# Kernel tuning notes

Measured on AMD Instinct MI355X. Metric: run time of the kernel, lower is better.

Reference implementation:

```python
import jax, jax.numpy as jnp
import numpy as np

T, H, F, E, K = 1024, 1024, 2048, 8, 2  # tokens, hidden, ffn_inter, experts, top_k


def setup_inputs() -> dict:
    key = jax.random.key(0)
    ks = jax.random.split(key, 7)
    return {
        "hidden_states": jax.random.normal(ks[0], (T, H), dtype=jnp.float32),
        "token_selected_experts": jax.random.randint(ks[1], (T, K), 0, E, dtype=jnp.int32),
        "token_final_scales": jax.random.uniform(ks[2], (T, K), dtype=jnp.float32),
        "w1": jax.random.normal(ks[3], (E, 2 * F, H), dtype=jnp.float32) * 0.02,  # gated fc1: [gate; linear]
        "b1": jax.random.normal(ks[4], (E, 2 * F), dtype=jnp.float32) * 0.02,
        "w2": jax.random.normal(ks[5], (E, H, F), dtype=jnp.float32) * 0.02,
        "b2": jax.random.normal(ks[6], (E, H), dtype=jnp.float32) * 0.02,
    }


def reference(hidden_states, token_selected_experts, token_final_scales, w1, b1, w2, b2):
    # Grouped GEMM fc1 over all experts: [T, E, 2F]
    h1 = jnp.einsum('th,efh->tef', hidden_states, w1) + b1[None]
    ffn = w2.shape[2]
    gate, lin = h1[..., :ffn], h1[..., ffn:]
    act = jax.nn.silu(gate) * lin                      # swiglu gated activation, [T, E, F]
    y_all = jnp.einsum('tef,ehf->teh', act, w2) + b2[None]  # fc2, [T, E, H]
    # Gather the top-k selected experts per token and combine with final scales
    sel = token_selected_experts.astype(jnp.int32)     # [T, K]
    y_sel = jnp.take_along_axis(y_all, sel[:, :, None], axis=1)  # [T, K, H]
    out = jnp.sum(y_sel * token_final_scales[:, :, None], axis=1)  # [T, H]
    return out
```

## Files before the change

### kernel.cpp

```cpp
#include <hip/hip_runtime.h>
#include <hip/hip_bf16.h>
#include <cstdint>
#include <cstddef>

#define TDIM 1024
#define HDIM 1024
#define FDIM 2048
#define NEXP 8
#define NENT 2048

typedef __bf16 bf16_t;
typedef __bf16 bf16x4 __attribute__((ext_vector_type(4)));
typedef __bf16 bf16x8 __attribute__((ext_vector_type(8)));
typedef float  f32x4  __attribute__((ext_vector_type(4)));

#define H_ELEMS ((size_t)TDIM*HDIM)

#define WB_OFFSETS 0
#define WB_ETOK    64
#define WB_ESCALE  (WB_ETOK + NENT*4)
#define WB_ACT     16512
#define WB_H       (WB_ACT + (size_t)NENT*FDIM*2)

__device__ __forceinline__ void gload16(const void* g, void* l) {
  __builtin_amdgcn_global_load_lds((const __attribute__((address_space(1))) void*)g,
                                   (__attribute__((address_space(3))) void*)l, 16, 0, 0);
}

__device__ __forceinline__ bf16x8 cvt8(const float4 a, const float4 b) {
  bf16x8 o;
  o[0]=(bf16_t)a.x; o[1]=(bf16_t)a.y; o[2]=(bf16_t)a.z; o[3]=(bf16_t)a.w;
  o[4]=(bf16_t)b.x; o[5]=(bf16_t)b.y; o[6]=(bf16_t)b.z; o[7]=(bf16_t)b.w;
  return o;
}

__global__ void route_all(const int* __restrict__ sel, const float* __restrict__ scal,
                          int* __restrict__ offsets, int* __restrict__ etok,
                          float* __restrict__ escale) {
  __shared__ int cnt[NEXP], cnt2[NEXP], offs[NEXP+1];
  const int t = threadIdx.x;
  if (t < NEXP) { cnt[t] = 0; cnt2[t] = 0; }
  __syncthreads();
  int e8[8];
  #pragma unroll
  for (int q = 0; q < 8; q++) {
    int i = t*8 + q;
    e8[q] = sel[i];
    atomicAdd(&cnt[e8[q]], 1);
  }
  __syncthreads();
  if (t == 0) {
    int s = 0;
    for (int e = 0; e < NEXP; e++) { offs[e] = s; offsets[e] = s; s += cnt[e]; }
    offs[NEXP] = s; offsets[NEXP] = s;
  }
  __syncthreads();
  #pragma unroll
  for (int q = 0; q < 8; q++) {
    int i = t*8 + q;
    int e = e8[q];
    int pos = offs[e] + atomicAdd(&cnt2[e], 1);
    etok[pos]   = i >> 1;
    escale[pos] = scal[i];
  }
}

__global__ void convert_h(const float* __restrict__ h, bf16_t* __restrict__ hbf) {
  size_t idx = ((size_t)blockIdx.x*256 + threadIdx.x) * 8;
  float4 v0 = ((const float4*)(h + idx))[0];
  float4 v1 = ((const float4*)(h + idx))[1];
  *(bf16x8*)(hbf + idx) = cvt8(v0, v1);
}


__global__ __launch_bounds__(256, 3) void gemm1_v5(
    const bf16_t* __restrict__ hbf, const float* __restrict__ w1,
    const float* __restrict__ b1, const int* __restrict__ offsets,
    const int* __restrict__ etok, bf16_t* __restrict__ act)
{
  const int e   = blockIdx.z;
  const int off = offsets[e];
  const int nt  = offsets[e+1] - off;
  const int m0  = blockIdx.y * 128;
  if (m0 >= nt) return;
  const int n0  = blockIdx.x * 64;

  __shared__ __align__(16) bf16_t As[128*32];
  __shared__ __align__(16) bf16_t Bg[64*32];
  __shared__ __align__(16) bf16_t Bl[64*32];

  const int tid  = threadIdx.x;
  const int w    = tid >> 6, lane = tid & 63;
  const int quad = lane >> 4, lr = lane & 15;
  const int wm   = w >> 1,  wn = w & 1;

  const bf16_t* asrc[2];
  bf16_t* adst[2];
  #pragma unroll
  for (int i = 0; i < 2; i++) {
    const int row = i*64 + w*16 + (lane >> 2);
    const int seg = (lane & 3) ^ (row & 3);
    int ent = m0 + row; if (ent > nt-1) ent = nt-1;
    const int tok = etok[off + ent];
    asrc[i] = hbf + (size_t)tok*HDIM + seg*8;
    adst[i] = &As[(i*64 + w*16)*32];
  }

  const int br = tid >> 2, bs = tid & 3;
  const float* gsrc = w1 + ((size_t)e*2*FDIM + (size_t)(n0 + br))*HDIM + bs*8;
  const float* lsrc = gsrc + (size_t)FDIM*HDIM;
  const int bofs = br*32 + ((bs ^ (br & 3)) << 3);

  const int aswz = (quad ^ (lr & 3)) << 3;
  int aoff[4], boff[2];
  #pragma unroll
  for (int i = 0; i < 4; i++) aoff[i] = (wm*64 + i*16 + lr)*32 + aswz;
  #pragma unroll
  for (int j = 0; j < 2; j++) boff[j] = (wn*32 + j*16 + lr)*32 + aswz;

  f32x4 accg[4][2] = {}, accl[4][2] = {};

  float4 g4[2], l4[2];
  { const float4* p = (const float4*)gsrc; g4[0]=p[0]; g4[1]=p[1];
    const float4* q = (const float4*)lsrc; l4[0]=q[0]; l4[1]=q[1]; }

  for (int k0 = 0; k0 < HDIM; k0 += 32) {
    __syncthreads();
    gload16(asrc[0] + k0, adst[0]);
    gload16(asrc[1] + k0, adst[1]);
    *(bf16x8*)&Bg[bofs] = cvt8(g4[0], g4[1]);
    *(bf16x8*)&Bl[bofs] = cvt8(l4[0], l4[1]);
    __syncthreads();

    if (k0 + 32 < HDIM) {
      const float4* p = (const float4*)(gsrc + k0 + 32); g4[0]=p[0]; g4[1]=p[1];
      const float4* q = (const float4*)(lsrc + k0 + 32); l4[0]=q[0]; l4[1]=q[1];
    }

    bf16x8 af[4], gf[2], lf[2];
    #pragma unroll
    for (int i = 0; i < 4; i++) af[i] = *(const bf16x8*)&As[aoff[i]];
    #pragma unroll
    for (int j = 0; j < 2; j++) {
      gf[j] = *(const bf16x8*)&Bg[boff[j]];
      lf[j] = *(const bf16x8*)&Bl[boff[j]];
    }
    #pragma unroll
    for (int i = 0; i < 4; i++)
      #pragma unroll
      for (int j = 0; j < 2; j++) {
        accg[i][j] = __builtin_amdgcn_mfma_f32_16x16x32_bf16(af[i], gf[j], accg[i][j], 0, 0, 0);
        accl[i][j] = __builtin_amdgcn_mfma_f32_16x16x32_bf16(af[i], lf[j], accl[i][j], 0, 0, 0);
      }
  }

  #pragma unroll
  for (int j = 0; j < 2; j++) {
    const int f = n0 + wn*32 + j*16 + lr;
    const float bg_ = b1[e*2*FDIM + f];
    const float bl_ = b1[e*2*FDIM + FDIM + f];
    #pragma unroll
    for (int i = 0; i < 4; i++) {
      #pragma unroll
      for (int r = 0; r < 4; r++) {
        const int m = wm*64 + i*16 + quad*4 + r;
        if (m0 + m < nt) {
          const float g = accg[i][j][r] + bg_;
          const float l = accl[i][j][r] + bl_;
          const float s = g / (1.f + __expf(-g)) * l;
          act[(size_t)(off + m0 + m)*FDIM + f] = (bf16_t)s;
        }
      }
    }
  }
}

__global__ __launch_bounds__(256, 3) void gemm2_v5(
    const bf16_t* __restrict__ act, const float* __restrict__ w2,
    const float* __restrict__ b2, const int* __restrict__ offsets,
    const int* __restrict__ etok, const float* __restrict__ escale,
    float* __restrict__ out)
{
  const int e   = blockIdx.z;
  const int off = offsets[e];
  const int nt  = offsets[e+1] - off;
  const int m0  = blockIdx.y * 128;
  if (m0 >= nt) return;
  const int n0  = (blockIdx.x >> 2) * 128;
  const int kc  = blockIdx.x & 3;
  const int kbeg = kc * (FDIM/4);

  __shared__ __align__(16) bf16_t As[128*32];
  __shared__ __align__(16) bf16_t Bs[128*32];

  const int tid  = threadIdx.x;
  const int w    = tid >> 6, lane = tid & 63;
  const int quad = lane >> 4, lr = lane & 15;
  const int wm   = w >> 1,  wn = w & 1;

  const bf16_t* asrc[2];
  bf16_t* adst[2];
  #pragma unroll
  for (int i = 0; i < 2; i++) {
    const int row = i*64 + w*16 + (lane >> 2);
    const int seg = (lane & 3) ^ (row & 3);
    int ent = m0 + row; if (ent > nt-1) ent = nt-1;
    asrc[i] = act + (size_t)(off + ent)*FDIM + kbeg + seg*8;
    adst[i] = &As[(i*64 + w*16)*32];
  }

  const int br = tid >> 1, bc = tid & 1;
  const float* bsrc = w2 + ((size_t)e*HDIM + (size_t)(n0 + br))*FDIM + kbeg + bc*16;
  const int bofs0 = br*32 + (((2*bc)   ^ (br & 3)) << 3);
  const int bofs1 = br*32 + (((2*bc+1) ^ (br & 3)) << 3);

  const int aswz = (quad ^ (lr & 3)) << 3;
  int aoff[4], boff[4];
  #pragma unroll
  for (int i = 0; i < 4; i++) aoff[i] = (wm*64 + i*16 + lr)*32 + aswz;
  #pragma unroll
  for (int j = 0; j < 4; j++) boff[j] = (wn*64 + j*16 + lr)*32 + aswz;

  f32x4 acc[4][4] = {};

  float4 b4[4];
  { const float4* p = (const float4*)bsrc;
    b4[0]=p[0]; b4[1]=p[1]; b4[2]=p[2]; b4[3]=p[3]; }

  for (int k0 = 0; k0 < FDIM/4; k0 += 32) {
    __syncthreads();
    gload16(asrc[0] + k0, adst[0]);
    gload16(asrc[1] + k0, adst[1]);
    *(bf16x8*)&Bs[bofs0] = cvt8(b4[0], b4[1]);
    *(bf16x8*)&Bs[bofs1] = cvt8(b4[2], b4[3]);
    __syncthreads();

    if (k0 + 32 < FDIM/4) {
      const float4* p = (const float4*)(bsrc + k0 + 32);
      b4[0]=p[0]; b4[1]=p[1]; b4[2]=p[2]; b4[3]=p[3];
    }

    bf16x8 af[4], bfr[4];
    #pragma unroll
    for (int i = 0; i < 4; i++) af[i] = *(const bf16x8*)&As[aoff[i]];
    #pragma unroll
    for (int j = 0; j < 4; j++) bfr[j] = *(const bf16x8*)&Bs[boff[j]];
    #pragma unroll
    for (int i = 0; i < 4; i++)
      #pragma unroll
      for (int j = 0; j < 4; j++)
        acc[i][j] = __builtin_amdgcn_mfma_f32_16x16x32_bf16(af[i], bfr[j], acc[i][j], 0, 0, 0);
  }

  #pragma unroll
  for (int i = 0; i < 4; i++) {
    #pragma unroll
    for (int r = 0; r < 4; r++) {
      const int m = wm*64 + i*16 + quad*4 + r;
      if (m0 + m < nt) {
        const int slot = off + m0 + m;
        const int t    = etok[slot];
        const float s  = escale[slot];
        #pragma unroll
        for (int j = 0; j < 4; j++) {
          const int n = n0 + wn*64 + j*16 + lr;
          float v = acc[i][j][r];
          if (kc == 0) v += b2[e*HDIM + n];
          atomicAdd(&out[(size_t)t*HDIM + n], s * v);
        }
      }
    }
  }
}

extern "C" void kernel_launch(void* const* d_in, const int* in_sizes, int n_in,
                              void* d_out, int out_size, void* d_ws, size_t ws_size,
                              hipStream_t stream) {
  const float* hidden = (const float*)d_in[0];
  const int*   sel    = (const int*)d_in[1];
  const float* scal   = (const float*)d_in[2];
  const float* w1     = (const float*)d_in[3];
  const float* b1     = (const float*)d_in[4];
  const float* w2     = (const float*)d_in[5];
  const float* b2     = (const float*)d_in[6];
  float* out = (float*)d_out;

  char* ws = (char*)d_ws;
  int*    offsets = (int*)(ws + WB_OFFSETS);
  int*    etok    = (int*)(ws + WB_ETOK);
  float*  escale  = (float*)(ws + WB_ESCALE);
  bf16_t* act     = (bf16_t*)(ws + WB_ACT);
  bf16_t* hbf     = (bf16_t*)(ws + WB_H);

  hipMemsetAsync(d_out, 0, (size_t)out_size * sizeof(float), stream);

  route_all<<<1, 256, 0, stream>>>(sel, scal, offsets, etok, escale);
  convert_h<<<(int)(H_ELEMS/8/256), 256, 0, stream>>>(hidden, hbf);

  gemm1_v5<<<dim3(FDIM/64, NENT/128, NEXP), 256, 0, stream>>>(hbf, w1, b1, offsets, etok, act);
  gemm2_v5<<<dim3((HDIM/128)*4, NENT/128, NEXP), 256, 0, stream>>>(act, w2, b2, offsets, etok, escale, out);
}
```

Baseline: 334.6 us.

## Double-buffer LDS tiles in both expert GEMMs with one barrier per step

Both grouped GEMM kernels now keep two LDS buffers for the A and B tiles. The next tile is staged (async global-to-LDS for activations, converted fp32 weights for B) while MFMAs run on the current one, and the two __syncthreads per k-step become a single s_barrier with explicit waitcnt and sched_barrier fences. The LDS swizzle also gains an extra XOR term on (row>>2)&3 to reduce bank conflicts. LDS use doubles, which may limit residency at 3 blocks per CU, and the hand-written vmcnt counts must match the issued loads exactly.

Measured after the change: 341.9 us. +2.2%, slower.

```diff
diff --git a/kernel.cpp b/kernel.cpp
--- a/kernel.cpp
+++ b/kernel.cpp
@@ -32,6 +32,10 @@
   o[0]=(bf16_t)a.x; o[1]=(bf16_t)a.y; o[2]=(bf16_t)a.z; o[3]=(bf16_t)a.w;
   o[4]=(bf16_t)b.x; o[5]=(bf16_t)b.y; o[6]=(bf16_t)b.z; o[7]=(bf16_t)b.w;
   return o;
+}
+
+__device__ __forceinline__ int segswz(int seg, int row) {
+  return seg ^ (row & 3) ^ ((row >> 2) & 3);
 }
 
 __global__ void route_all(const int* __restrict__ sel, const float* __restrict__ scal,
@@ -73,7 +77,7 @@
 }
 
 
-__global__ __launch_bounds__(256, 3) void gemm1_v5(
+__global__ __launch_bounds__(256, 3) void gemm1_v6(
     const bf16_t* __restrict__ hbf, const float* __restrict__ w1,
     const float* __restrict__ b1, const int* __restrict__ offsets,
     const int* __restrict__ etok, bf16_t* __restrict__ act)
@@ -85,74 +89,121 @@
   if (m0 >= nt) return;
   const int n0  = blockIdx.x * 64;
 
-  __shared__ __align__(16) bf16_t As[128*32];
-  __shared__ __align__(16) bf16_t Bg[64*32];
-  __shared__ __align__(16) bf16_t Bl[64*32];
+  __shared__ __align__(16) bf16_t As[2][128*32];
+  __shared__ __align__(16) bf16_t Bg[2][64*32];
+  __shared__ __align__(16) bf16_t Bl[2][64*32];
 
   const int tid  = threadIdx.x;
   const int w    = tid >> 6, lane = tid & 63;
   const int quad = lane >> 4, lr = lane & 15;
   const int wm   = w >> 1,  wn = w & 1;
 
-  const bf16_t* asrc[2];
-  bf16_t* adst[2];
-  #pragma unroll
-  for (int i = 0; i < 2; i++) {
-    const int row = i*64 + w*16 + (lane >> 2);
-    const int seg = (lane & 3) ^ (row & 3);
-    int ent = m0 + row; if (ent > nt-1) ent = nt-1;
-    const int tok = etok[off + ent];
-    asrc[i] = hbf + (size_t)tok*HDIM + seg*8;
-    adst[i] = &As[(i*64 + w*16)*32];
+  const bf16_t* asrc0; const bf16_t* asrc1;
+  int arow0, arow1;
+  {
+    const int r0 = 0*64 + w*16 + (lane >> 2);
+    const int r1 = 1*64 + w*16 + (lane >> 2);
+    const int s0 = segswz(lane & 3, r0);
+    const int s1 = segswz(lane & 3, r1);
+    int e0 = m0 + r0; if (e0 > nt-1) e0 = nt-1;
+    int e1 = m0 + r1; if (e1 > nt-1) e1 = nt-1;
+    asrc0 = hbf + (size_t)etok[off + e0]*HDIM + s0*8;
+    asrc1 = hbf + (size_t)etok[off + e1]*HDIM + s1*8;
+    arow0 = (0*64 + w*16)*32;
+    arow1 = (1*64 + w*16)*32;
   }
 
   const int br = tid >> 2, bs = tid & 3;
   const float* gsrc = w1 + ((size_t)e*2*FDIM + (size_t)(n0 + br))*HDIM + bs*8;
   const float* lsrc = gsrc + (size_t)FDIM*HDIM;
-  const int bofs = br*32 + ((bs ^ (br & 3)) << 3);
-
-  const int aswz = (quad ^ (lr & 3)) << 3;
+  const int bofs = br*32 + (segswz(bs, br) << 3);
+
   int aoff[4], boff[2];
   #pragma unroll
-  for (int i = 0; i < 4; i++) aoff[i] = (wm*64 + i*16 + lr)*32 + aswz;
-  #pragma unroll
-  for (int j = 0; j < 2; j++) boff[j] = (wn*32 + j*16 + lr)*32 + aswz;
+  for (int i = 0; i < 4; i++) {
+    const int r = wm*64 + i*16 + lr;
+    aoff[i] = r*32 + (segswz(quad, r) << 3);
+  }
+  #pragma unroll
+  for (int j = 0; j < 2; j++) {
+    const int r = wn*32 + j*16 + lr;
+    boff[j] = r*32 + (segswz(quad, r) << 3);
+  }
 
   f32x4 accg[4][2] = {}, accl[4][2] = {};
-
   float4 g4[2], l4[2];
-  { const float4* p = (const float4*)gsrc; g4[0]=p[0]; g4[1]=p[1];
-    const float4* q = (const float4*)lsrc; l4[0]=q[0]; l4[1]=q[1]; }
-
-  for (int k0 = 0; k0 < HDIM; k0 += 32) {
-    __syncthreads();
-    gload16(asrc[0] + k0, adst[0]);
-    gload16(asrc[1] + k0, adst[1]);
-    *(bf16x8*)&Bg[bofs] = cvt8(g4[0], g4[1]);
-    *(bf16x8*)&Bl[bofs] = cvt8(l4[0], l4[1]);
-    __syncthreads();
-
-    if (k0 + 32 < HDIM) {
-      const float4* p = (const float4*)(gsrc + k0 + 32); g4[0]=p[0]; g4[1]=p[1];
-      const float4* q = (const float4*)(lsrc + k0 + 32); l4[0]=q[0]; l4[1]=q[1];
-    }
-
-    bf16x8 af[4], gf[2], lf[2];
-    #pragma unroll
-    for (int i = 0; i < 4; i++) af[i] = *(const bf16x8*)&As[aoff[i]];
-    #pragma unroll
-    for (int j = 0; j < 2; j++) {
-      gf[j] = *(const bf16x8*)&Bg[boff[j]];
-      lf[j] = *(const bf16x8*)&Bl[boff[j]];
-    }
-    #pragma unroll
-    for (int i = 0; i < 4; i++)
-      #pragma unroll
-      for (int j = 0; j < 2; j++) {
-        accg[i][j] = __builtin_amdgcn_mfma_f32_16x16x32_bf16(af[i], gf[j], accg[i][j], 0, 0, 0);
-        accl[i][j] = __builtin_amdgcn_mfma_f32_16x16x32_bf16(af[i], lf[j], accl[i][j], 0, 0, 0);
-      }
-  }
+
+#define G1_LOADB(K0)                                                          \
+  { const float4* p_ = (const float4*)(gsrc + (K0)); g4[0]=p_[0]; g4[1]=p_[1];\
+    const float4* q_ = (const float4*)(lsrc + (K0)); l4[0]=q_[0]; l4[1]=q_[1]; }
+
+#define G1_STAGE(K0, NXT)                                                     \
+  { *(bf16x8*)&Bg[NXT][bofs] = cvt8(g4[0], g4[1]);                            \
+    *(bf16x8*)&Bl[NXT][bofs] = cvt8(l4[0], l4[1]);                            \
+    __builtin_amdgcn_sched_barrier(0);                                        \
+    gload16(asrc0 + (K0), &As[NXT][arow0]);                                   \
+    gload16(asrc1 + (K0), &As[NXT][arow1]);                                   \
+    __builtin_amdgcn_sched_barrier(0); }
+
+#define G1_MFMA(CUR)                                                          \
+  { bf16x8 af[4], gf[2], lf[2];                                               \
+    _Pragma("unroll")                                                         \
+    for (int i = 0; i < 4; i++) af[i] = *(const bf16x8*)&As[CUR][aoff[i]];    \
+    _Pragma("unroll")                                                         \
+    for (int j = 0; j < 2; j++) {                                             \
+      gf[j] = *(const bf16x8*)&Bg[CUR][boff[j]];                              \
+      lf[j] = *(const bf16x8*)&Bl[CUR][boff[j]];                              \
+    }                                                                         \
+    _Pragma("unroll")                                                         \
+    for (int i = 0; i < 4; i++)                                               \
+      _Pragma("unroll")                                                       \
+      for (int j = 0; j < 2; j++) {                                           \
+        accg[i][j] = __builtin_amdgcn_mfma_f32_16x16x32_bf16(af[i], gf[j], accg[i][j], 0, 0, 0); \
+        accl[i][j] = __builtin_amdgcn_mfma_f32_16x16x32_bf16(af[i], lf[j], accl[i][j], 0, 0, 0); \
+      } }
+
+  G1_LOADB(0);
+  __builtin_amdgcn_sched_barrier(0);
+  gload16(asrc0 + 0, &As[0][arow0]);
+  gload16(asrc1 + 0, &As[0][arow1]);
+  __builtin_amdgcn_sched_barrier(0);
+  *(bf16x8*)&Bg[0][bofs] = cvt8(g4[0], g4[1]);
+  *(bf16x8*)&Bl[0][bofs] = cvt8(l4[0], l4[1]);
+  G1_LOADB(32);
+  asm volatile("s_waitcnt vmcnt(4) lgkmcnt(0)" ::: "memory");
+  __builtin_amdgcn_sched_barrier(0);
+  __builtin_amdgcn_s_barrier();
+  __builtin_amdgcn_sched_barrier(0);
+
+#define G1_STEP_FULL(CUR)                                                     \
+  { G1_STAGE(k0 + 32, (CUR)^1);                                               \
+    G1_LOADB(k0 + 64);                                                        \
+    __builtin_amdgcn_sched_barrier(0);                                        \
+    G1_MFMA(CUR);                                                             \
+    asm volatile("s_waitcnt vmcnt(4) lgkmcnt(0)" ::: "memory");               \
+    __builtin_amdgcn_sched_barrier(0);                                        \
+    __builtin_amdgcn_s_barrier();                                             \
+    __builtin_amdgcn_sched_barrier(0);                                        \
+    k0 += 32; }
+
+  int k0 = 0;
+  while (k0 < HDIM - 64) {
+    G1_STEP_FULL(0);
+    G1_STEP_FULL(1);
+  }
+  G1_STAGE(992, 1);
+  __builtin_amdgcn_sched_barrier(0);
+  G1_MFMA(0);
+  asm volatile("s_waitcnt vmcnt(0) lgkmcnt(0)" ::: "memory");
+  __builtin_amdgcn_sched_barrier(0);
+  __builtin_amdgcn_s_barrier();
+  __builtin_amdgcn_sched_barrier(0);
+  G1_MFMA(1);
+
+#undef G1_STEP_FULL
+#undef G1_MFMA
+#undef G1_STAGE
+#undef G1_LOADB
 
   #pragma unroll
   for (int j = 0; j < 2; j++) {
@@ -175,7 +226,7 @@
   }
 }
 
-__global__ __launch_bounds__(256, 3) void gemm2_v5(
+__global__ __launch_bounds__(256, 3) void gemm2_v6(
     const bf16_t* __restrict__ act, const float* __restrict__ w2,
     const float* __restrict__ b2, const int* __restrict__ offsets,
     const int* __restrict__ etok, const float* __restrict__ escale,
@@ -190,67 +241,115 @@
   const int kc  = blockIdx.x & 3;
   const int kbeg = kc * (FDIM/4);
 
-  __shared__ __align__(16) bf16_t As[128*32];
-  __shared__ __align__(16) bf16_t Bs[128*32];
+  __shared__ __align__(16) bf16_t As[2][128*32];
+  __shared__ __align__(16) bf16_t Bs[2][128*32];
 
   const int tid  = threadIdx.x;
   const int w    = tid >> 6, lane = tid & 63;
   const int quad = lane >> 4, lr = lane & 15;
   const int wm   = w >> 1,  wn = w & 1;
 
-  const bf16_t* asrc[2];
-  bf16_t* adst[2];
-  #pragma unroll
-  for (int i = 0; i < 2; i++) {
-    const int row = i*64 + w*16 + (lane >> 2);
-    const int seg = (lane & 3) ^ (row & 3);
-    int ent = m0 + row; if (ent > nt-1) ent = nt-1;
-    asrc[i] = act + (size_t)(off + ent)*FDIM + kbeg + seg*8;
-    adst[i] = &As[(i*64 + w*16)*32];
+  const bf16_t* asrc0; const bf16_t* asrc1;
+  int arow0, arow1;
+  {
+    const int r0 = 0*64 + w*16 + (lane >> 2);
+    const int r1 = 1*64 + w*16 + (lane >> 2);
+    const int s0 = segswz(lane & 3, r0);
+    const int s1 = segswz(lane & 3, r1);
+    int e0 = m0 + r0; if (e0 > nt-1) e0 = nt-1;
+    int e1 = m0 + r1; if (e1 > nt-1) e1 = nt-1;
+    asrc0 = act + (size_t)(off + e0)*FDIM + kbeg + s0*8;
+    asrc1 = act + (size_t)(off + e1)*FDIM + kbeg + s1*8;
+    arow0 = (0*64 + w*16)*32;
+    arow1 = (1*64 + w*16)*32;
   }
 
   const int br = tid >> 1, bc = tid & 1;
   const float* bsrc = w2 + ((size_t)e*HDIM + (size_t)(n0 + br))*FDIM + kbeg + bc*16;
-  const int bofs0 = br*32 + (((2*bc)   ^ (br & 3)) << 3);
-  const int bofs1 = br*32 + (((2*bc+1) ^ (br & 3)) << 3);
-
-  const int aswz = (quad ^ (lr & 3)) << 3;
+  const int bofs0 = br*32 + (segswz(2*bc,   br) << 3);
+  const int bofs1 = br*32 + (segswz(2*bc+1, br) << 3);
+
   int aoff[4], boff[4];
   #pragma unroll
-  for (int i = 0; i < 4; i++) aoff[i] = (wm*64 + i*16 + lr)*32 + aswz;
-  #pragma unroll
-  for (int j = 0; j < 4; j++) boff[j] = (wn*64 + j*16 + lr)*32 + aswz;
+  for (int i = 0; i < 4; i++) {
+    const int r = wm*64 + i*16 + lr;
+    aoff[i] = r*32 + (segswz(quad, r) << 3);
+  }
+  #pragma unroll
+  for (int j = 0; j < 4; j++) {
+    const int r = wn*64 + j*16 + lr;
+    boff[j] = r*32 + (segswz(quad, r) << 3);
+  }
 
   f32x4 acc[4][4] = {};
-
   float4 b4[4];
-  { const float4* p = (const float4*)bsrc;
-    b4[0]=p[0]; b4[1]=p[1]; b4[2]=p[2]; b4[3]=p[3]; }
-
-  for (int k0 = 0; k0 < FDIM/4; k0 += 32) {
-    __syncthreads();
-    gload16(asrc[0] + k0, adst[0]);
-    gload16(asrc[1] + k0, adst[1]);
-    *(bf16x8*)&Bs[bofs0] = cvt8(b4[0], b4[1]);
-    *(bf16x8*)&Bs[bofs1] = cvt8(b4[2], b4[3]);
-    __syncthreads();
-
-    if (k0 + 32 < FDIM/4) {
-      const float4* p = (const float4*)(bsrc + k0 + 32);
-      b4[0]=p[0]; b4[1]=p[1]; b4[2]=p[2]; b4[3]=p[3];
-    }
-
-    bf16x8 af[4], bfr[4];
-    #pragma unroll
-    for (int i = 0; i < 4; i++) af[i] = *(const bf16x8*)&As[aoff[i]];
-    #pragma unroll
-    for (int j = 0; j < 4; j++) bfr[j] = *(const bf16x8*)&Bs[boff[j]];
-    #pragma unroll
-    for (int i = 0; i < 4; i++)
-      #pragma unroll
-      for (int j = 0; j < 4; j++)
-        acc[i][j] = __builtin_amdgcn_mfma_f32_16x16x32_bf16(af[i], bfr[j], acc[i][j], 0, 0, 0);
-  }
+
+#define G2_LOADB(K0)                                                          \
+  { const float4* p_ = (const float4*)(bsrc + (K0));                          \
+    b4[0]=p_[0]; b4[1]=p_[1]; b4[2]=p_[2]; b4[3]=p_[3]; }
+
+#define G2_STAGE(K0, NXT)                                                     \
+  { *(bf16x8*)&Bs[NXT][bofs0] = cvt8(b4[0], b4[1]);                           \
+    *(bf16x8*)&Bs[NXT][bofs1] = cvt8(b4[2], b4[3]);                           \
+    __builtin_amdgcn_sched_barrier(0);                                        \
+    gload16(asrc0 + (K0), &As[NXT][arow0]);                                   \
+    gload16(asrc1 + (K0), &As[NXT][arow1]);                                   \
+    __builtin_amdgcn_sched_barrier(0); }
+
+#define G2_MFMA(CUR)                                                          \
+  { bf16x8 af[4], bfr[4];                                                     \
+    _Pragma("unroll")                                                         \
+    for (int i = 0; i < 4; i++) af[i] = *(const bf16x8*)&As[CUR][aoff[i]];    \
+    _Pragma("unroll")                                                         \
+    for (int j = 0; j < 4; j++) bfr[j] = *(const bf16x8*)&Bs[CUR][boff[j]];   \
+    _Pragma("unroll")                                                         \
+    for (int i = 0; i < 4; i++)                                               \
+      _Pragma("unroll")                                                       \
+      for (int j = 0; j < 4; j++)                                             \
+        acc[i][j] = __builtin_amdgcn_mfma_f32_16x16x32_bf16(af[i], bfr[j], acc[i][j], 0, 0, 0); }
+
+  G2_LOADB(0);
+  __builtin_amdgcn_sched_barrier(0);
+  gload16(asrc0 + 0, &As[0][arow0]);
+  gload16(asrc1 + 0, &As[0][arow1]);
+  __builtin_amdgcn_sched_barrier(0);
+  *(bf16x8*)&Bs[0][bofs0] = cvt8(b4[0], b4[1]);
+  *(bf16x8*)&Bs[0][bofs1] = cvt8(b4[2], b4[3]);
+  G2_LOADB(32);
+  asm volatile("s_waitcnt vmcnt(4) lgkmcnt(0)" ::: "memory");
+  __builtin_amdgcn_sched_barrier(0);
+  __builtin_amdgcn_s_barrier();
+  __builtin_amdgcn_sched_barrier(0);
+
+#define G2_STEP_FULL(CUR)                                                     \
+  { G2_STAGE(k0 + 32, (CUR)^1);                                               \
+    G2_LOADB(k0 + 64);                                                        \
+    __builtin_amdgcn_sched_barrier(0);                                        \
+    G2_MFMA(CUR);                                                             \
+    asm volatile("s_waitcnt vmcnt(4) lgkmcnt(0)" ::: "memory");               \
+    __builtin_amdgcn_sched_barrier(0);                                        \
+    __builtin_amdgcn_s_barrier();                                             \
+    __builtin_amdgcn_sched_barrier(0);                                        \
+    k0 += 32; }
+
+  int k0 = 0;
+  while (k0 < FDIM/4 - 64) {
+    G2_STEP_FULL(0);
+    G2_STEP_FULL(1);
+  }
+  G2_STAGE(480, 1);
+  __builtin_amdgcn_sched_barrier(0);
+  G2_MFMA(0);
+  asm volatile("s_waitcnt vmcnt(0) lgkmcnt(0)" ::: "memory");
+  __builtin_amdgcn_sched_barrier(0);
+  __builtin_amdgcn_s_barrier();
+  __builtin_amdgcn_sched_barrier(0);
+  G2_MFMA(1);
+
+#undef G2_STEP_FULL
+#undef G2_MFMA
+#undef G2_STAGE
+#undef G2_LOADB
 
   #pragma unroll
   for (int i = 0; i < 4; i++) {
@@ -297,6 +396,6 @@
   route_all<<<1, 256, 0, stream>>>(sel, scal, offsets, etok, escale);
   convert_h<<<(int)(H_ELEMS/8/256), 256, 0, stream>>>(hidden, hbf);
 
-  gemm1_v5<<<dim3(FDIM/64, NENT/128, NEXP), 256, 0, stream>>>(hbf, w1, b1, offsets, etok, act);
-  gemm2_v5<<<dim3((HDIM/128)*4, NENT/128, NEXP), 256, 0, stream>>>(act, w2, b2, offsets, etok, escale, out);
-}
+  gemm1_v6<<<dim3(FDIM/64, NENT/128, NEXP), 256, 0, stream>>>(hbf, w1, b1, offsets, etok, act);
+  gemm2_v6<<<dim3((HDIM/128)*4, NENT/128, NEXP), 256, 0, stream>>>(act, w2, b2, offsets, etok, escale, out);
+}
```
